# Optimization experiments

Hardware: AMD Instinct MI355X
Metric: run time of the kernel (lower is better)

The kernel has to match this reference:

```python
import jax, jax.numpy as jnp
import numpy as np

EPS = 1e-8
N = 4
B = 1_000_000


def setup_inputs() -> dict:
    key = jax.random.key(0)
    g = jax.random.normal(key, (B, N, N), dtype=jnp.float32)
    # SPD covariance-like matrices: G G^T + 0.1 I (well-conditioned, distinct eigvals)
    x = jnp.einsum('bik,bjk->bij', g, g) / N + 0.1 * jnp.eye(N, dtype=jnp.float32)
    return {"x": x}


def reference(x):
    # 1) symmetrize + epsilon regularization (ensure SPD)
    sym = 0.5 * (x + jnp.swapaxes(x, -1, -2)) + EPS * jnp.eye(N, dtype=x.dtype)
    # 2) exact matrix log via eigendecomposition
    w, v = jnp.linalg.eigh(sym)                      # w: [B, N], v: [B, N, N]
    log_w = jnp.log(jnp.maximum(w, EPS))
    logm = jnp.einsum('bik,bk,bjk->bij', v, log_w, v)  # V diag(log w) V^T
    # 3) re-symmetrize
    logm = 0.5 * (logm + jnp.swapaxes(logm, -1, -2))
    # 4) upper-triangular vectorization, row-major (i, j>=i) order
    iu, ju = jnp.triu_indices(N)
    return logm[:, iu, ju]                           # [B, N*(N+1)//2]
```

## Files before the change

kernel.cpp:

```cpp
#include <hip/hip_runtime.h>
#include <math.h>

#ifndef NSWEEP
#define NSWEEP 4
#endif

#define EPSV 1e-8f
#define NM 3
#define BT 256
#define MPB (NM * BT)

__device__ __forceinline__ float fast_rsqf(float x) {
#if __has_builtin(__builtin_amdgcn_rsqf)
  return __builtin_amdgcn_rsqf(x);
#else
  return rsqrtf(x);
#endif
}
__device__ __forceinline__ float fast_logf(float x) {
#if __has_builtin(__builtin_amdgcn_logf)
  return __builtin_amdgcn_logf(x) * 0.6931471805599453f;
#else
  return logf(x);
#endif
}

#define JROT(APP, AQQ, APQ, AK1P, AK1Q, AK2P, AK2Q,                         \
             VP0, VQ0, VP1, VQ1, VP2, VQ2, VP3, VQ3)                        \
  do {                                                                      \
    float aa_ = APQ;                                                        \
    float d_ = AQQ - APP;                                                   \
    float a2_ = aa_ + aa_;                                                  \
    float r2_ = fmaf(d_, d_, a2_ * a2_);                                    \
    float h_ = fast_rsqf(fmaxf(r2_, 1e-30f));                               \
    float p_ = fabsf(d_) * h_;                                              \
    p_ = (r2_ <= 1e-30f) ? 1.0f : p_;                                       \
    float q_ = fmaf(2.0f, p_, 2.0f);                                        \
    float ri_ = fast_rsqf(q_);                                              \
    float c_ = q_ * (0.5f * ri_);                                           \
    float n_ = __int_as_float(__float_as_int(a2_ * h_) ^                    \
                              (__float_as_int(d_) & 0x80000000));           \
    float s_ = n_ * ri_;                                                    \
    float t_ = (n_ + n_) * (ri_ * ri_);                                     \
    float ta_ = t_ * aa_;                                                   \
    APP = APP - ta_;                                                        \
    AQQ = AQQ + ta_;                                                        \
    APQ = 0.0f;                                                             \
    { float kp_ = AK1P, kq_ = AK1Q;                                         \
      AK1P = fmaf(c_, kp_, -s_ * kq_);                                      \
      AK1Q = fmaf(s_, kp_, c_ * kq_); }                                     \
    { float kp_ = AK2P, kq_ = AK2Q;                                         \
      AK2P = fmaf(c_, kp_, -s_ * kq_);                                      \
      AK2Q = fmaf(s_, kp_, c_ * kq_); }                                     \
    { float p0_ = VP0, q0_ = VQ0;                                           \
      VP0 = fmaf(c_, p0_, -s_ * q0_);                                       \
      VQ0 = fmaf(s_, p0_, c_ * q0_); }                                      \
    { float p0_ = VP1, q0_ = VQ1;                                           \
      VP1 = fmaf(c_, p0_, -s_ * q0_);                                       \
      VQ1 = fmaf(s_, p0_, c_ * q0_); }                                      \
    { float p0_ = VP2, q0_ = VQ2;                                           \
      VP2 = fmaf(c_, p0_, -s_ * q0_);                                       \
      VQ2 = fmaf(s_, p0_, c_ * q0_); }                                      \
    { float p0_ = VP3, q0_ = VQ3;                                           \
      VP3 = fmaf(c_, p0_, -s_ * q0_);                                       \
      VQ3 = fmaf(s_, p0_, c_ * q0_); }                                      \
  } while (0)

#define ROT_01(m) JROT(A[m][0], A[m][4], A[m][1], A[m][2], A[m][5],         \
                       A[m][3], A[m][6], V[m][0], V[m][1], V[m][4],         \
                       V[m][5], V[m][8], V[m][9], V[m][12], V[m][13])
#define ROT_02(m) JROT(A[m][0], A[m][7], A[m][2], A[m][1], A[m][5],         \
                       A[m][3], A[m][8], V[m][0], V[m][2], V[m][4],         \
                       V[m][6], V[m][8], V[m][10], V[m][12], V[m][14])
#define ROT_03(m) JROT(A[m][0], A[m][9], A[m][3], A[m][1], A[m][6],         \
                       A[m][2], A[m][8], V[m][0], V[m][3], V[m][4],         \
                       V[m][7], V[m][8], V[m][11], V[m][12], V[m][15])
#define ROT_12(m) JROT(A[m][4], A[m][7], A[m][5], A[m][1], A[m][2],         \
                       A[m][6], A[m][8], V[m][1], V[m][2], V[m][5],         \
                       V[m][6], V[m][9], V[m][10], V[m][13], V[m][14])
#define ROT_13(m) JROT(A[m][4], A[m][9], A[m][6], A[m][1], A[m][3],         \
                       A[m][5], A[m][8], V[m][1], V[m][3], V[m][5],         \
                       V[m][7], V[m][9], V[m][11], V[m][13], V[m][15])
#define ROT_23(m) JROT(A[m][7], A[m][9], A[m][8], A[m][2], A[m][3],         \
                       A[m][5], A[m][6], V[m][2], V[m][3], V[m][6],         \
                       V[m][7], V[m][10], V[m][11], V[m][14], V[m][15])

__global__ __launch_bounds__(256, 4) void TangentSpaceLayer_64141041598486_kernel(
    const float* __restrict__ x, float* __restrict__ out, int B) {
  __shared__ __align__(16) float so[BT * 10];
  const int t = threadIdx.x;
  const int base = blockIdx.x * MPB;

  float A[NM][10];
  float V[NM][16];

#pragma unroll
  for (int m = 0; m < NM; ++m) {
    const int idx = min(base + m * BT + t, B - 1);
    const float4* p = (const float4*)(x + (size_t)idx * 16);
    float4 r0 = p[0], r1 = p[1], r2 = p[2], r3 = p[3];
    A[m][0] = r0.x + EPSV;
    A[m][1] = 0.5f * (r0.y + r1.x);
    A[m][2] = 0.5f * (r0.z + r2.x);
    A[m][3] = 0.5f * (r0.w + r3.x);
    A[m][4] = r1.y + EPSV;
    A[m][5] = 0.5f * (r1.z + r2.y);
    A[m][6] = 0.5f * (r1.w + r3.y);
    A[m][7] = r2.z + EPSV;
    A[m][8] = 0.5f * (r2.w + r3.z);
    A[m][9] = r3.w + EPSV;
#pragma unroll
    for (int i = 0; i < 16; ++i) V[m][i] = (i % 5 == 0) ? 1.0f : 0.0f;
  }

#pragma unroll 1
  for (int sweep = 0; sweep < NSWEEP; ++sweep) {
#pragma unroll
    for (int m = 0; m < NM; ++m) ROT_01(m);
#pragma unroll
    for (int m = 0; m < NM; ++m) ROT_02(m);
#pragma unroll
    for (int m = 0; m < NM; ++m) ROT_03(m);
#pragma unroll
    for (int m = 0; m < NM; ++m) ROT_12(m);
#pragma unroll
    for (int m = 0; m < NM; ++m) ROT_13(m);
#pragma unroll
    for (int m = 0; m < NM; ++m) ROT_23(m);
  }

#pragma unroll
  for (int m = 0; m < NM; ++m) {
    float lw0 = fast_logf(fmaxf(A[m][0], EPSV));
    float lw1 = fast_logf(fmaxf(A[m][4], EPSV));
    float lw2 = fast_logf(fmaxf(A[m][7], EPSV));
    float lw3 = fast_logf(fmaxf(A[m][9], EPSV));

    float w00 = V[m][0] * lw0, w01 = V[m][1] * lw1, w02 = V[m][2] * lw2,
          w03 = V[m][3] * lw3;
    float w10 = V[m][4] * lw0, w11 = V[m][5] * lw1, w12 = V[m][6] * lw2,
          w13 = V[m][7] * lw3;
    float w20 = V[m][8] * lw0, w21 = V[m][9] * lw1, w22 = V[m][10] * lw2,
          w23 = V[m][11] * lw3;
    float w30 = V[m][12] * lw0, w31 = V[m][13] * lw1, w32 = V[m][14] * lw2,
          w33 = V[m][15] * lw3;

    float* sp = so + t * 10;
    sp[0] = fmaf(w00, V[m][0], fmaf(w01, V[m][1], fmaf(w02, V[m][2], w03 * V[m][3])));
    sp[1] = fmaf(w00, V[m][4], fmaf(w01, V[m][5], fmaf(w02, V[m][6], w03 * V[m][7])));
    sp[2] = fmaf(w00, V[m][8], fmaf(w01, V[m][9], fmaf(w02, V[m][10], w03 * V[m][11])));
    sp[3] = fmaf(w00, V[m][12], fmaf(w01, V[m][13], fmaf(w02, V[m][14], w03 * V[m][15])));
    sp[4] = fmaf(w10, V[m][4], fmaf(w11, V[m][5], fmaf(w12, V[m][6], w13 * V[m][7])));
    sp[5] = fmaf(w10, V[m][8], fmaf(w11, V[m][9], fmaf(w12, V[m][10], w13 * V[m][11])));
    sp[6] = fmaf(w10, V[m][12], fmaf(w11, V[m][13], fmaf(w12, V[m][14], w13 * V[m][15])));
    sp[7] = fmaf(w20, V[m][8], fmaf(w21, V[m][9], fmaf(w22, V[m][10], w23 * V[m][11])));
    sp[8] = fmaf(w20, V[m][12], fmaf(w21, V[m][13], fmaf(w22, V[m][14], w23 * V[m][15])));
    sp[9] = fmaf(w30, V[m][12], fmaf(w31, V[m][13], fmaf(w32, V[m][14], w33 * V[m][15])));

    __syncthreads();

    const int mbase = base + m * BT;
    const int valid = min(BT, B - mbase);
    const int nf = valid * 10;
    const int n4 = nf >> 2;
    float* obase = out + (size_t)mbase * 10;
    const float4* s4 = (const float4*)so;
    float4* o4 = (float4*)obase;
    for (int i = t; i < n4; i += BT) o4[i] = s4[i];
    for (int i = n4 * 4 + t; i < nf; i += BT) obase[i] = so[i];

    __syncthreads();
  }
}

extern "C" void kernel_launch(void* const* d_in, const int* in_sizes, int n_in,
                              void* d_out, int out_size, void* d_ws, size_t ws_size,
                              hipStream_t stream) {
  const float* x = (const float*)d_in[0];
  float* out = (float*)d_out;
  const int B = in_sizes[0] / 16;
  const int blocks = (B + MPB - 1) / MPB;
  hipLaunchKernelGGL(TangentSpaceLayer_64141041598486_kernel, dim3(blocks),
                     dim3(BT), 0, stream, x, out, B);
}
```

Measured before the change: 120.7 us.

## Process two matrices per thread as paired floats for packed-math Jacobi

Replaces the three-matrices-per-thread layout with two matrices per thread, held in float pairs so the compiler can emit packed FP32 (v_pk_fma/v_pk_mul) instructions for the Jacobi rotations and reconstruction. Each block now covers 512 matrices instead of 768, so the grid has more blocks. This cuts per-matrix instruction count if packing happens, but lowers per-thread ILP and relies on the compiler actually packing the struct operations. The rsqrt and log calls stay scalar.

```diff
diff --git a/kernel.cpp b/kernel.cpp
--- a/kernel.cpp
+++ b/kernel.cpp
@@ -6,9 +6,8 @@
 #endif
 
 #define EPSV 1e-8f
-#define NM 3
 #define BT 256
-#define MPB (NM * BT)
+#define MPB (2 * BT)
 
 __device__ __forceinline__ float fast_rsqf(float x) {
 #if __has_builtin(__builtin_amdgcn_rsqf)
@@ -25,141 +24,142 @@
 #endif
 }
 
+struct f2 { float x, y; };
+__device__ __forceinline__ f2 F2(float a, float b) { f2 r; r.x = a; r.y = b; return r; }
+__device__ __forceinline__ f2 f2add(f2 a, f2 b) { return F2(a.x + b.x, a.y + b.y); }
+__device__ __forceinline__ f2 f2sub(f2 a, f2 b) { return F2(a.x - b.x, a.y - b.y); }
+__device__ __forceinline__ f2 f2mul(f2 a, f2 b) { return F2(a.x * b.x, a.y * b.y); }
+__device__ __forceinline__ f2 f2muls(f2 a, float s) { return F2(a.x * s, a.y * s); }
+__device__ __forceinline__ f2 f2fma(f2 a, f2 b, f2 c) {
+  return F2(fmaf(a.x, b.x, c.x), fmaf(a.y, b.y, c.y));
+}
+__device__ __forceinline__ f2 f2rsq(f2 a) { return F2(fast_rsqf(a.x), fast_rsqf(a.y)); }
+__device__ __forceinline__ f2 f2abs(f2 a) { return F2(fabsf(a.x), fabsf(a.y)); }
+__device__ __forceinline__ f2 f2maxs(f2 a, float s) { return F2(fmaxf(a.x, s), fmaxf(a.y, s)); }
+__device__ __forceinline__ f2 f2log(f2 a) { return F2(fast_logf(fmaxf(a.x, EPSV)), fast_logf(fmaxf(a.y, EPSV))); }
+__device__ __forceinline__ f2 f2neg(f2 a) { return F2(-a.x, -a.y); }
+__device__ __forceinline__ f2 f2sgnx(f2 mag, f2 sgn) {
+  return F2(__int_as_float(__float_as_int(mag.x) ^ (__float_as_int(sgn.x) & 0x80000000)),
+            __int_as_float(__float_as_int(mag.y) ^ (__float_as_int(sgn.y) & 0x80000000)));
+}
+__device__ __forceinline__ f2 f2selp(f2 r2, f2 p) {
+  return F2(r2.x <= 1e-30f ? 1.0f : p.x, r2.y <= 1e-30f ? 1.0f : p.y);
+}
+
+#define ROTP_(P, Q)                                   \
+  { f2 p0_ = P, q0_ = Q;                              \
+    P = f2fma(c_, p0_, f2mul(ns_, q0_));              \
+    Q = f2fma(s_, p0_, f2mul(c_, q0_)); }
+
 #define JROT(APP, AQQ, APQ, AK1P, AK1Q, AK2P, AK2Q,                         \
              VP0, VQ0, VP1, VQ1, VP2, VQ2, VP3, VQ3)                        \
   do {                                                                      \
-    float aa_ = APQ;                                                        \
-    float d_ = AQQ - APP;                                                   \
-    float a2_ = aa_ + aa_;                                                  \
-    float r2_ = fmaf(d_, d_, a2_ * a2_);                                    \
-    float h_ = fast_rsqf(fmaxf(r2_, 1e-30f));                               \
-    float p_ = fabsf(d_) * h_;                                              \
-    p_ = (r2_ <= 1e-30f) ? 1.0f : p_;                                       \
-    float q_ = fmaf(2.0f, p_, 2.0f);                                        \
-    float ri_ = fast_rsqf(q_);                                              \
-    float c_ = q_ * (0.5f * ri_);                                           \
-    float n_ = __int_as_float(__float_as_int(a2_ * h_) ^                    \
-                              (__float_as_int(d_) & 0x80000000));           \
-    float s_ = n_ * ri_;                                                    \
-    float t_ = (n_ + n_) * (ri_ * ri_);                                     \
-    float ta_ = t_ * aa_;                                                   \
-    APP = APP - ta_;                                                        \
-    AQQ = AQQ + ta_;                                                        \
-    APQ = 0.0f;                                                             \
-    { float kp_ = AK1P, kq_ = AK1Q;                                         \
-      AK1P = fmaf(c_, kp_, -s_ * kq_);                                      \
-      AK1Q = fmaf(s_, kp_, c_ * kq_); }                                     \
-    { float kp_ = AK2P, kq_ = AK2Q;                                         \
-      AK2P = fmaf(c_, kp_, -s_ * kq_);                                      \
-      AK2Q = fmaf(s_, kp_, c_ * kq_); }                                     \
-    { float p0_ = VP0, q0_ = VQ0;                                           \
-      VP0 = fmaf(c_, p0_, -s_ * q0_);                                       \
-      VQ0 = fmaf(s_, p0_, c_ * q0_); }                                      \
-    { float p0_ = VP1, q0_ = VQ1;                                           \
-      VP1 = fmaf(c_, p0_, -s_ * q0_);                                       \
-      VQ1 = fmaf(s_, p0_, c_ * q0_); }                                      \
-    { float p0_ = VP2, q0_ = VQ2;                                           \
-      VP2 = fmaf(c_, p0_, -s_ * q0_);                                       \
-      VQ2 = fmaf(s_, p0_, c_ * q0_); }                                      \
-    { float p0_ = VP3, q0_ = VQ3;                                           \
-      VP3 = fmaf(c_, p0_, -s_ * q0_);                                       \
-      VQ3 = fmaf(s_, p0_, c_ * q0_); }                                      \
+    f2 aa_ = APQ;                                                           \
+    f2 d_ = f2sub(AQQ, APP);                                                \
+    f2 a2_ = f2add(aa_, aa_);                                               \
+    f2 r2_ = f2fma(d_, d_, f2mul(a2_, a2_));                                \
+    f2 h_ = f2rsq(f2maxs(r2_, 1e-30f));                                     \
+    f2 p_ = f2selp(r2_, f2mul(f2abs(d_), h_));                              \
+    f2 q_ = F2(fmaf(2.0f, p_.x, 2.0f), fmaf(2.0f, p_.y, 2.0f));             \
+    f2 ri_ = f2rsq(q_);                                                     \
+    f2 c_ = f2mul(q_, f2muls(ri_, 0.5f));                                   \
+    f2 n_ = f2sgnx(f2mul(a2_, h_), d_);                                     \
+    f2 s_ = f2mul(n_, ri_);                                                 \
+    f2 ns_ = f2neg(s_);                                                     \
+    f2 t_ = f2mul(f2add(n_, n_), f2mul(ri_, ri_));                          \
+    f2 ta_ = f2mul(t_, aa_);                                                \
+    APP = f2sub(APP, ta_);                                                  \
+    AQQ = f2add(AQQ, ta_);                                                  \
+    APQ = F2(0.0f, 0.0f);                                                   \
+    ROTP_(AK1P, AK1Q)                                                       \
+    ROTP_(AK2P, AK2Q)                                                       \
+    ROTP_(VP0, VQ0)                                                         \
+    ROTP_(VP1, VQ1)                                                         \
+    ROTP_(VP2, VQ2)                                                         \
+    ROTP_(VP3, VQ3)                                                         \
   } while (0)
 
-#define ROT_01(m) JROT(A[m][0], A[m][4], A[m][1], A[m][2], A[m][5],         \
-                       A[m][3], A[m][6], V[m][0], V[m][1], V[m][4],         \
-                       V[m][5], V[m][8], V[m][9], V[m][12], V[m][13])
-#define ROT_02(m) JROT(A[m][0], A[m][7], A[m][2], A[m][1], A[m][5],         \
-                       A[m][3], A[m][8], V[m][0], V[m][2], V[m][4],         \
-                       V[m][6], V[m][8], V[m][10], V[m][12], V[m][14])
-#define ROT_03(m) JROT(A[m][0], A[m][9], A[m][3], A[m][1], A[m][6],         \
-                       A[m][2], A[m][8], V[m][0], V[m][3], V[m][4],         \
-                       V[m][7], V[m][8], V[m][11], V[m][12], V[m][15])
-#define ROT_12(m) JROT(A[m][4], A[m][7], A[m][5], A[m][1], A[m][2],         \
-                       A[m][6], A[m][8], V[m][1], V[m][2], V[m][5],         \
-                       V[m][6], V[m][9], V[m][10], V[m][13], V[m][14])
-#define ROT_13(m) JROT(A[m][4], A[m][9], A[m][6], A[m][1], A[m][3],         \
-                       A[m][5], A[m][8], V[m][1], V[m][3], V[m][5],         \
-                       V[m][7], V[m][9], V[m][11], V[m][13], V[m][15])
-#define ROT_23(m) JROT(A[m][7], A[m][9], A[m][8], A[m][2], A[m][3],         \
-                       A[m][5], A[m][6], V[m][2], V[m][3], V[m][6],         \
-                       V[m][7], V[m][10], V[m][11], V[m][14], V[m][15])
+#define ROT_01 JROT(A[0], A[4], A[1], A[2], A[5], A[3], A[6],               \
+                    V[0], V[1], V[4], V[5], V[8], V[9], V[12], V[13])
+#define ROT_02 JROT(A[0], A[7], A[2], A[1], A[5], A[3], A[8],               \
+                    V[0], V[2], V[4], V[6], V[8], V[10], V[12], V[14])
+#define ROT_03 JROT(A[0], A[9], A[3], A[1], A[6], A[2], A[8],               \
+                    V[0], V[3], V[4], V[7], V[8], V[11], V[12], V[15])
+#define ROT_12 JROT(A[4], A[7], A[5], A[1], A[2], A[6], A[8],               \
+                    V[1], V[2], V[5], V[6], V[9], V[10], V[13], V[14])
+#define ROT_13 JROT(A[4], A[9], A[6], A[1], A[3], A[5], A[8],               \
+                    V[1], V[3], V[5], V[7], V[9], V[11], V[13], V[15])
+#define ROT_23 JROT(A[7], A[9], A[8], A[2], A[3], A[5], A[6],               \
+                    V[2], V[3], V[6], V[7], V[10], V[11], V[14], V[15])
 
 __global__ __launch_bounds__(256, 4) void TangentSpaceLayer_64141041598486_kernel(
     const float* __restrict__ x, float* __restrict__ out, int B) {
   __shared__ __align__(16) float so[BT * 10];
   const int t = threadIdx.x;
   const int base = blockIdx.x * MPB;
+  const int i0 = min(base + t, B - 1);
+  const int i1 = min(base + BT + t, B - 1);
 
-  float A[NM][10];
-  float V[NM][16];
+  const float4* p0 = (const float4*)(x + (size_t)i0 * 16);
+  const float4* p1 = (const float4*)(x + (size_t)i1 * 16);
+  float4 a0 = p0[0], a1 = p0[1], a2 = p0[2], a3 = p0[3];
+  float4 b0 = p1[0], b1 = p1[1], b2 = p1[2], b3 = p1[3];
 
+  f2 A[10], V[16];
+  A[0] = F2(a0.x + EPSV, b0.x + EPSV);
+  A[1] = F2(0.5f * (a0.y + a1.x), 0.5f * (b0.y + b1.x));
+  A[2] = F2(0.5f * (a0.z + a2.x), 0.5f * (b0.z + b2.x));
+  A[3] = F2(0.5f * (a0.w + a3.x), 0.5f * (b0.w + b3.x));
+  A[4] = F2(a1.y + EPSV, b1.y + EPSV);
+  A[5] = F2(0.5f * (a1.z + a2.y), 0.5f * (b1.z + b2.y));
+  A[6] = F2(0.5f * (a1.w + a3.y), 0.5f * (b1.w + b3.y));
+  A[7] = F2(a2.z + EPSV, b2.z + EPSV);
+  A[8] = F2(0.5f * (a2.w + a3.z), 0.5f * (b2.w + b3.z));
+  A[9] = F2(a3.w + EPSV, b3.w + EPSV);
 #pragma unroll
-  for (int m = 0; m < NM; ++m) {
-    const int idx = min(base + m * BT + t, B - 1);
-    const float4* p = (const float4*)(x + (size_t)idx * 16);
-    float4 r0 = p[0], r1 = p[1], r2 = p[2], r3 = p[3];
-    A[m][0] = r0.x + EPSV;
-    A[m][1] = 0.5f * (r0.y + r1.x);
-    A[m][2] = 0.5f * (r0.z + r2.x);
-    A[m][3] = 0.5f * (r0.w + r3.x);
-    A[m][4] = r1.y + EPSV;
-    A[m][5] = 0.5f * (r1.z + r2.y);
-    A[m][6] = 0.5f * (r1.w + r3.y);
-    A[m][7] = r2.z + EPSV;
-    A[m][8] = 0.5f * (r2.w + r3.z);
-    A[m][9] = r3.w + EPSV;
-#pragma unroll
-    for (int i = 0; i < 16; ++i) V[m][i] = (i % 5 == 0) ? 1.0f : 0.0f;
-  }
+  for (int i = 0; i < 16; ++i) V[i] = F2((i % 5 == 0) ? 1.0f : 0.0f,
+                                         (i % 5 == 0) ? 1.0f : 0.0f);
 
 #pragma unroll 1
   for (int sweep = 0; sweep < NSWEEP; ++sweep) {
-#pragma unroll
-    for (int m = 0; m < NM; ++m) ROT_01(m);
-#pragma unroll
-    for (int m = 0; m < NM; ++m) ROT_02(m);
-#pragma unroll
-    for (int m = 0; m < NM; ++m) ROT_03(m);
-#pragma unroll
-    for (int m = 0; m < NM; ++m) ROT_12(m);
-#pragma unroll
-    for (int m = 0; m < NM; ++m) ROT_13(m);
-#pragma unroll
-    for (int m = 0; m < NM; ++m) ROT_23(m);
+    ROT_01; ROT_02; ROT_03; ROT_12; ROT_13; ROT_23;
   }
 
+  f2 lw0 = f2log(A[0]);
+  f2 lw1 = f2log(A[4]);
+  f2 lw2 = f2log(A[7]);
+  f2 lw3 = f2log(A[9]);
+
+  f2 w00 = f2mul(V[0], lw0),  w01 = f2mul(V[1], lw1),
+     w02 = f2mul(V[2], lw2),  w03 = f2mul(V[3], lw3);
+  f2 w10 = f2mul(V[4], lw0),  w11 = f2mul(V[5], lw1),
+     w12 = f2mul(V[6], lw2),  w13 = f2mul(V[7], lw3);
+  f2 w20 = f2mul(V[8], lw0),  w21 = f2mul(V[9], lw1),
+     w22 = f2mul(V[10], lw2), w23 = f2mul(V[11], lw3);
+  f2 w30 = f2mul(V[12], lw0), w31 = f2mul(V[13], lw1),
+     w32 = f2mul(V[14], lw2), w33 = f2mul(V[15], lw3);
+
+  f2 o[10];
+  o[0] = f2fma(w00, V[0],  f2fma(w01, V[1],  f2fma(w02, V[2],  f2mul(w03, V[3]))));
+  o[1] = f2fma(w00, V[4],  f2fma(w01, V[5],  f2fma(w02, V[6],  f2mul(w03, V[7]))));
+  o[2] = f2fma(w00, V[8],  f2fma(w01, V[9],  f2fma(w02, V[10], f2mul(w03, V[11]))));
+  o[3] = f2fma(w00, V[12], f2fma(w01, V[13], f2fma(w02, V[14], f2mul(w03, V[15]))));
+  o[4] = f2fma(w10, V[4],  f2fma(w11, V[5],  f2fma(w12, V[6],  f2mul(w13, V[7]))));
+  o[5] = f2fma(w10, V[8],  f2fma(w11, V[9],  f2fma(w12, V[10], f2mul(w13, V[11]))));
+  o[6] = f2fma(w10, V[12], f2fma(w11, V[13], f2fma(w12, V[14], f2mul(w13, V[15]))));
+  o[7] = f2fma(w20, V[8],  f2fma(w21, V[9],  f2fma(w22, V[10], f2mul(w23, V[11]))));
+  o[8] = f2fma(w20, V[12], f2fma(w21, V[13], f2fma(w22, V[14], f2mul(w23, V[15]))));
+  o[9] = f2fma(w30, V[12], f2fma(w31, V[13], f2fma(w32, V[14], f2mul(w33, V[15]))));
+
+#pragma unroll 1
+  for (int half = 0; half < 2; ++half) {
+    float* sp = so + t * 10;
 #pragma unroll
-  for (int m = 0; m < NM; ++m) {
-    float lw0 = fast_logf(fmaxf(A[m][0], EPSV));
-    float lw1 = fast_logf(fmaxf(A[m][4], EPSV));
-    float lw2 = fast_logf(fmaxf(A[m][7], EPSV));
-    float lw3 = fast_logf(fmaxf(A[m][9], EPSV));
-
-    float w00 = V[m][0] * lw0, w01 = V[m][1] * lw1, w02 = V[m][2] * lw2,
-          w03 = V[m][3] * lw3;
-    float w10 = V[m][4] * lw0, w11 = V[m][5] * lw1, w12 = V[m][6] * lw2,
-          w13 = V[m][7] * lw3;
-    float w20 = V[m][8] * lw0, w21 = V[m][9] * lw1, w22 = V[m][10] * lw2,
-          w23 = V[m][11] * lw3;
-    float w30 = V[m][12] * lw0, w31 = V[m][13] * lw1, w32 = V[m][14] * lw2,
-          w33 = V[m][15] * lw3;
-
-    float* sp = so + t * 10;
-    sp[0] = fmaf(w00, V[m][0], fmaf(w01, V[m][1], fmaf(w02, V[m][2], w03 * V[m][3])));
-    sp[1] = fmaf(w00, V[m][4], fmaf(w01, V[m][5], fmaf(w02, V[m][6], w03 * V[m][7])));
-    sp[2] = fmaf(w00, V[m][8], fmaf(w01, V[m][9], fmaf(w02, V[m][10], w03 * V[m][11])));
-    sp[3] = fmaf(w00, V[m][12], fmaf(w01, V[m][13], fmaf(w02, V[m][14], w03 * V[m][15])));
-    sp[4] = fmaf(w10, V[m][4], fmaf(w11, V[m][5], fmaf(w12, V[m][6], w13 * V[m][7])));
-    sp[5] = fmaf(w10, V[m][8], fmaf(w11, V[m][9], fmaf(w12, V[m][10], w13 * V[m][11])));
-    sp[6] = fmaf(w10, V[m][12], fmaf(w11, V[m][13], fmaf(w12, V[m][14], w13 * V[m][15])));
-    sp[7] = fmaf(w20, V[m][8], fmaf(w21, V[m][9], fmaf(w22, V[m][10], w23 * V[m][11])));
-    sp[8] = fmaf(w20, V[m][12], fmaf(w21, V[m][13], fmaf(w22, V[m][14], w23 * V[m][15])));
-    sp[9] = fmaf(w30, V[m][12], fmaf(w31, V[m][13], fmaf(w32, V[m][14], w33 * V[m][15])));
+    for (int i = 0; i < 10; ++i) sp[i] = half ? o[i].y : o[i].x;
 
     __syncthreads();
 
-    const int mbase = base + m * BT;
+    const int mbase = base + half * BT;
     const int valid = min(BT, B - mbase);
     const int nf = valid * 10;
     const int n4 = nf >> 2;
```

New measurement: 111.9 us. 7.3% less time.
